# Performance work log

Hardware: AMD Instinct MI355X
Metric: run time of the kernel (lower is better)

The kernel has to match this reference:

```python
import jax, jax.numpy as jnp
import numpy as np

OBS = 128; N_AGENT = 16; N_ACTION = 8; N_LAYER = 2; HID = 128
GE = 256; LE = 256; F1 = 512; F2 = 512


def _edges(batch_size, n):
    # all ordered pairs (i, j), i != j, within each sample; GCNConv adds self-loops
    i, j = np.meshgrid(np.arange(n), np.arange(n), indexing='ij')
    m = i != j
    src0, dst0 = i[m], j[m]                      # [n*(n-1)]
    off = (np.arange(batch_size) * n)[:, None]
    src = (src0[None, :] + off).reshape(-1)
    dst = (dst0[None, :] + off).reshape(-1)
    return jnp.asarray(src, jnp.int32), jnp.asarray(dst, jnp.int32)


def setup_inputs() -> dict:
    key = jax.random.key(0)
    ks = jax.random.split(key, 16)
    g = lambda k, shp, fan: jax.random.normal(k, shp, jnp.float32) / np.sqrt(fan)
    return {
        'obs_j': jax.random.normal(ks[0], (2048, N_AGENT, OBS), jnp.float32),
        'W_pre': g(ks[1], (OBS, HID), OBS), 'b_pre': jnp.zeros((HID,), jnp.float32),
        'W_gcn': g(ks[2], (N_LAYER, HID, HID), HID), 'b_gcn': jnp.zeros((N_LAYER, HID), jnp.float32),
        'W_post': g(ks[3], (HID, GE), HID), 'b_post': jnp.zeros((GE,), jnp.float32),
        'W_loc': g(ks[4], (OBS, LE), OBS), 'b_loc': jnp.zeros((LE,), jnp.float32),
        'W1': g(ks[5], (GE + LE, F1), GE + LE), 'b1': jnp.zeros((F1,), jnp.float32),
        'W2': g(ks[6], (F1, F2), F1), 'b2': jnp.zeros((F2,), jnp.float32),
        'W3': g(ks[7], (F2, N_ACTION), F2), 'b3': jnp.zeros((N_ACTION,), jnp.float32),
    }


def reference(obs_j, W_pre, b_pre, W_gcn, b_gcn, W_post, b_post,
              W_loc, b_loc, W1, b1, W2, b2, W3, b3):
    B, n, _ = obs_j.shape
    N = B * n
    obs = obs_j.reshape(N, OBS)
    x = jax.nn.relu(obs @ W_pre + b_pre)          # [N, HID]

    src, dst = _edges(B, n)
    # GCNConv with self-loops on a fully-connected graph: deg = n for every node,
    # edge norm = 1/sqrt(deg_i*deg_j) = 1/n for every (A+I) edge.
    inv_n = jnp.float32(1.0) / n
    for l in range(N_LAYER):
        h = x @ W_gcn[l]                          # lin (no bias inside propagate)
        agg = jax.ops.segment_sum(h[src], dst, num_segments=N)  # neighbor gather/scatter
        x = jax.nn.relu((agg + h) * inv_n + b_gcn[l])            # + self-loop msg, bias

    g = x.reshape(B, n, HID).mean(axis=1)         # global_mean_pool over each graph
    g = jax.nn.relu(g @ W_post + b_post)          # [B, GE]
    loc = jax.nn.relu(obs @ W_loc + b_loc)        # [B*n, LE]
    gi = jnp.repeat(g, n, axis=0)                 # repeat_interleave over agents
    z = jnp.concatenate([gi, loc], axis=1)
    z = jax.nn.relu(z @ W1 + b1)
    z = jax.nn.relu(z @ W2 + b2)
    q = z @ W3 + b3
    return q.reshape(B, n, N_ACTION)
```

## Files before the change

kernel.cpp:

```cpp
#include <hip/hip_runtime.h>
#include <hip/hip_bf16.h>
#include <stdint.h>

typedef __bf16 bf16;
typedef __bf16 bf16x4 __attribute__((ext_vector_type(4)));
typedef __bf16 bf16x8 __attribute__((ext_vector_type(8)));
typedef float f32x4 __attribute__((ext_vector_type(4)));

#define BM 128
#define BN 128
#define BK 64

#define GL(p) ((const __attribute__((address_space(1))) void*)(p))
#define SH(p) ((__attribute__((address_space(3))) void*)(p))

__device__ inline void tp(const float* W, bf16* WT, int id, int shiftK, int N) {
  int K = 1 << shiftK;
  int n = id >> shiftK;
  int k = id & (K - 1);
  WT[id] = (bf16)W[(size_t)k * N + n];
}

__global__ __launch_bounds__(256) void prep_all(
    const float* __restrict__ obs, bf16* __restrict__ obs_bf,
    const float* __restrict__ W1, const float* __restrict__ W2,
    bf16* __restrict__ W1T, bf16* __restrict__ W2T,
    const float* __restrict__ Wpre, const float* __restrict__ Wloc,
    const float* __restrict__ Wgcn, const float* __restrict__ Wpost,
    bf16* __restrict__ WpreLocT, bf16* __restrict__ Wg0T, bf16* __restrict__ Wg1T,
    bf16* __restrict__ WpostT,
    const float* __restrict__ bpre, const float* __restrict__ bloc,
    float* __restrict__ biasPL) {
  __shared__ bf16 tile[64 * 68];
  int blk = blockIdx.x;
  int tid = threadIdx.x;
  if (blk < 2048) {
    int id = blk * 256 + tid;
    const float4* s = (const float4*)(obs + (size_t)id * 8);
    float4 f0 = s[0], f1 = s[1];
    bf16x8 v;
    v[0] = (bf16)f0.x; v[1] = (bf16)f0.y; v[2] = (bf16)f0.z; v[3] = (bf16)f0.w;
    v[4] = (bf16)f1.x; v[5] = (bf16)f1.y; v[6] = (bf16)f1.z; v[7] = (bf16)f1.w;
    *(bf16x8*)(obs_bf + (size_t)id * 8) = v;
    return;
  }
  blk -= 2048;
  if (blk < 128) {
    const float* W = (blk < 64) ? W1 : W2;
    bf16* WT = (blk < 64) ? W1T : W2T;
    int t = blk & 63;
    int tk0 = (t >> 3) * 64, tn0 = (t & 7) * 64;
#pragma unroll
    for (int p = 0; p < 4; p++) {
      int kr = p * 16 + (tid >> 4), nc = (tid & 15) * 4;
      float4 f = *(const float4*)(W + (size_t)(tk0 + kr) * 512 + tn0 + nc);
      bf16x4 v; v[0] = (bf16)f.x; v[1] = (bf16)f.y; v[2] = (bf16)f.z; v[3] = (bf16)f.w;
      *(bf16x4*)&tile[kr * 68 + nc] = v;
    }
    __syncthreads();
#pragma unroll
    for (int p = 0; p < 4; p++) {
      int nr = p * 16 + (tid >> 4), kc = (tid & 15) * 4;
      bf16x4 v;
#pragma unroll
      for (int i = 0; i < 4; i++) v[i] = tile[(kc + i) * 68 + nr];
      *(bf16x4*)(WT + (size_t)(tn0 + nr) * 512 + tk0 + kc) = v;
    }
    return;
  }
  blk -= 128;
  if (blk < 448) {
    int id = blk * 256 + tid;
    if (id < 16384) { tp(Wpre, WpreLocT, id, 7, 128); return; } id -= 16384;
    if (id < 32768) { tp(Wloc, WpreLocT + 16384, id, 7, 256); return; } id -= 32768;
    if (id < 16384) { tp(Wgcn, Wg0T, id, 7, 128); return; } id -= 16384;
    if (id < 16384) { tp(Wgcn + 16384, Wg1T, id, 7, 128); return; } id -= 16384;
    tp(Wpost, WpostT, id, 7, 256);
    return;
  }
  if (tid < 128) biasPL[tid] = bpre[tid];
  biasPL[128 + tid] = bloc[tid];
}

template <int NT, bool CONCAT, bool POOL, bool QFUSE>
__global__ __launch_bounds__(256, 4) void gemm_k(
    const bf16* __restrict__ Ab, const bf16* __restrict__ Ag,
    const bf16* __restrict__ BT, const float* __restrict__ bias,
    bf16* __restrict__ C, int ldc, bf16* __restrict__ pool_out,
    const float* __restrict__ W3, float* __restrict__ qpart,
    int M, int K) {
  __shared__ bf16 smem[16384];
  bf16* As = smem;
  bf16* Bs = smem + 8192;

  const int tid = threadIdx.x;
  const int id = blockIdx.x;
  const int s = id >> 3;
  const int n_idx = s % NT;
  const int m0 = ((id & 7) + 8 * (s / NT)) * BM;
  const int n0 = n_idx * BN;

  f32x4 acc[4][4] = {};

  const int lane = tid & 63;
  const int wave = tid >> 6;
  const int wm = (wave >> 1) * 64;
  const int wn = (wave & 1) * 64;
  const int lm = lane & 15;
  const int quad = lane >> 4;

  for (int k0 = 0; k0 < K; k0 += BK) {
#pragma unroll
    for (int it = 0; it < 4; it++) {
      int idx = it * 256 + tid;
      int row = idx >> 3;
      int cv8 = (idx & 7) ^ (row & 7);
      int kk = k0 + cv8 * 8;
      const bf16* ga;
      if (CONCAT) {
        int r = m0 + row;
        ga = (k0 < 256) ? (Ag + (size_t)(r >> 4) * 256 + kk)
                        : (Ab + (size_t)r * 256 + (kk - 256));
      } else {
        ga = Ab + (size_t)(m0 + row) * K + kk;
      }
      const bf16* gb = BT + (size_t)(n0 + row) * K + kk;
      __builtin_amdgcn_global_load_lds(GL(ga), SH(&As[(idx & ~63) * 8]), 16, 0, 0);
      __builtin_amdgcn_global_load_lds(GL(gb), SH(&Bs[(idx & ~63) * 8]), 16, 0, 0);
    }
    __syncthreads();

#pragma unroll
    for (int ks = 0; ks < 2; ks++) {
      const int ua = quad + ks * 4;
      bf16x8 a[4], b[4];
#pragma unroll
      for (int i = 0; i < 4; i++) {
        int r = wm + lm + i * 16;
        a[i] = *(const bf16x8*)&As[r * 64 + ((ua ^ (r & 7)) * 8)];
      }
#pragma unroll
      for (int j = 0; j < 4; j++) {
        int r = wn + lm + j * 16;
        b[j] = *(const bf16x8*)&Bs[r * 64 + ((ua ^ (r & 7)) * 8)];
      }
#pragma unroll
      for (int i = 0; i < 4; i++)
#pragma unroll
        for (int j = 0; j < 4; j++)
          acc[i][j] = __builtin_amdgcn_mfma_f32_16x16x32_bf16(a[i], b[j], acc[i][j], 0, 0, 0);
    }
    __syncthreads();
  }

  if (POOL && n_idx == 0) {
#pragma unroll
    for (int i = 0; i < 4; i++) {
      int sample = (m0 + wm + i * 16) >> 4;
#pragma unroll
      for (int j = 0; j < 4; j++) {
        int col = wn + j * 16 + lm;
        float b = bias[col];
        float v = 0.f;
#pragma unroll
        for (int r = 0; r < 4; r++) v += fmaxf(acc[i][j][r] + b, 0.f);
        v += __shfl_xor(v, 16);
        v += __shfl_xor(v, 32);
        if (quad == 0) pool_out[(size_t)sample * 128 + col] = (bf16)(v * 0.0625f);
      }
    }
  } else if (QFUSE) {
#pragma unroll
    for (int i = 0; i < 4; i++)
#pragma unroll
      for (int j = 0; j < 4; j++) {
        int col = wn + j * 16 + lm;
        float b = bias[n0 + col];
#pragma unroll
        for (int r = 0; r < 4; r++) {
          int row = wm + i * 16 + quad * 4 + r;
          smem[row * 128 + col] = (bf16)fmaxf(acc[i][j][r] + b, 0.f);
        }
      }
    __syncthreads();
    int n = lane & 7;
    int kg = lane >> 3;
    float w3r[16];
#pragma unroll
    for (int i = 0; i < 16; i++) w3r[i] = W3[(size_t)(n0 + kg * 16 + i) * 8 + n];
    int rbase = wave * 32;
    for (int rr = 0; rr < 32; rr++) {
      const bf16* zr = &smem[(rbase + rr) * 128 + kg * 16];
      bf16x8 z0 = *(const bf16x8*)zr;
      bf16x8 z1v = *(const bf16x8*)(zr + 8);
      float v = 0.f;
#pragma unroll
      for (int i = 0; i < 8; i++) v += (float)z0[i] * w3r[i];
#pragma unroll
      for (int i = 0; i < 8; i++) v += (float)z1v[i] * w3r[8 + i];
      v += __shfl_down(v, 32);
      v += __shfl_down(v, 16);
      v += __shfl_down(v, 8);
      if (lane < 8) qpart[((size_t)n_idx * 32768 + m0 + rbase + rr) * 8 + n] = v;
    }
  } else {
#pragma unroll
    for (int i = 0; i < 4; i++)
#pragma unroll
      for (int j = 0; j < 4; j++) {
        int col = wn + j * 16 + lm;
        float b = bias[n0 + col];
#pragma unroll
        for (int r = 0; r < 4; r++) {
          int row = wm + i * 16 + quad * 4 + r;
          smem[row * 128 + col] = (bf16)fmaxf(acc[i][j][r] + b, 0.f);
        }
      }
    __syncthreads();
    const int coff = POOL ? (n0 - 128) : n0;
#pragma unroll
    for (int c = 0; c < 8; c++) {
      int ci = c * 256 + tid;
      int row = ci >> 4, col8 = (ci & 15) * 8;
      *(bf16x8*)&C[(size_t)(m0 + row) * ldc + coff + col8] = *(const bf16x8*)&smem[row * 128 + col8];
    }
  }
}

__global__ __launch_bounds__(256) void gcn_chain(
    const bf16* __restrict__ xbar, const bf16* __restrict__ Wg0T,
    const bf16* __restrict__ Wg1T, const bf16* __restrict__ WpostT,
    const float* __restrict__ b_gcn, const float* __restrict__ b_post,
    bf16* __restrict__ g) {
  __shared__ bf16 xs[16 * 136];
  __shared__ bf16 ws[256 * 136];
  const int tid = threadIdx.x;
  const int lane = tid & 63, wave = tid >> 6;
  const int lm = lane & 15, quad = lane >> 4;
  const int rb = blockIdx.x * 16;

  {
    int row = tid >> 4, cv = (tid & 15) * 8;
    *(bf16x8*)&xs[row * 136 + cv] = *(const bf16x8*)&xbar[(size_t)(rb + row) * 128 + cv];
  }

  const bf16* Wl[3] = {Wg0T, Wg1T, WpostT};
  const float* bl[3] = {b_gcn, b_gcn + 128, b_post};
  const int Nl[3] = {128, 128, 256};

  for (int l = 0; l < 3; l++) {
    const int N = Nl[l];
    __syncthreads();
    for (int c = tid; c < N * 16; c += 256) {
      int row = c >> 4, cv = (c & 15) * 8;
      *(bf16x8*)&ws[row * 136 + cv] = *(const bf16x8*)&Wl[l][(size_t)row * 128 + cv];
    }
    __syncthreads();
    const int nj = N / 64;
    f32x4 acc[4] = {};
#pragma unroll
    for (int kk = 0; kk < 128; kk += 32) {
      bf16x8 a = *(const bf16x8*)&xs[lm * 136 + quad * 8 + kk];
      for (int j = 0; j < nj; j++) {
        int col = (wave * nj + j) * 16 + lm;
        bf16x8 b = *(const bf16x8*)&ws[col * 136 + quad * 8 + kk];
        acc[j] = __builtin_amdgcn_mfma_f32_16x16x32_bf16(a, b, acc[j], 0, 0, 0);
      }
    }
    __syncthreads();
    const float* bias = bl[l];
    if (l < 2) {
      for (int j = 0; j < nj; j++) {
        int col = (wave * nj + j) * 16 + lm;
        float bv = bias[col];
#pragma unroll
        for (int r = 0; r < 4; r++)
          xs[(quad * 4 + r) * 136 + col] = (bf16)fmaxf(acc[j][r] + bv, 0.f);
      }
    } else {
      for (int j = 0; j < nj; j++) {
        int col = (wave * nj + j) * 16 + lm;
        float bv = bias[col];
#pragma unroll
        for (int r = 0; r < 4; r++)
          g[(size_t)(rb + quad * 4 + r) * 256 + col] = (bf16)fmaxf(acc[j][r] + bv, 0.f);
      }
    }
  }
}

__global__ __launch_bounds__(256) void reduce_q(const float* __restrict__ qpart,
                                                const float* __restrict__ b3,
                                                float* __restrict__ out) {
  int idx = blockIdx.x * 256 + threadIdx.x;
  const float4* qp = (const float4*)qpart;
  float4 v = qp[idx];
  float4 t1 = qp[idx + 65536];
  float4 t2 = qp[idx + 131072];
  float4 t3 = qp[idx + 196608];
  const float4* b = (const float4*)b3;
  float4 bb = b[idx & 1];
  v.x += t1.x + t2.x + t3.x + bb.x;
  v.y += t1.y + t2.y + t3.y + bb.y;
  v.z += t1.z + t2.z + t3.z + bb.z;
  v.w += t1.w + t2.w + t3.w + bb.w;
  ((float4*)out)[idx] = v;
}

extern "C" void kernel_launch(void* const* d_in, const int* in_sizes, int n_in,
                              void* d_out, int out_size, void* d_ws, size_t ws_size,
                              hipStream_t stream) {
  const float* obs    = (const float*)d_in[0];
  const float* W_pre  = (const float*)d_in[1];
  const float* b_pre  = (const float*)d_in[2];
  const float* W_gcn  = (const float*)d_in[3];
  const float* b_gcn  = (const float*)d_in[4];
  const float* W_post = (const float*)d_in[5];
  const float* b_post = (const float*)d_in[6];
  const float* W_loc  = (const float*)d_in[7];
  const float* b_loc  = (const float*)d_in[8];
  const float* W1     = (const float*)d_in[9];
  const float* b1     = (const float*)d_in[10];
  const float* W2     = (const float*)d_in[11];
  const float* b2     = (const float*)d_in[12];
  const float* W3     = (const float*)d_in[13];
  const float* b3     = (const float*)d_in[14];
  float* out = (float*)d_out;

  char* p = (char*)d_ws;
  auto alloc = [&](size_t bytes) { char* r = p; p += (bytes + 255) & ~(size_t)255; return r; };
  bf16* WpreLocT = (bf16*)alloc(384 * 128 * 2);
  float* biasPL  = (float*)alloc(384 * 4);
  bf16* Wg0T   = (bf16*)alloc(128 * 128 * 2);
  bf16* Wg1T   = (bf16*)alloc(128 * 128 * 2);
  bf16* WpostT = (bf16*)alloc(256 * 128 * 2);
  bf16* W1T    = (bf16*)alloc(512 * 512 * 2);
  bf16* W2T    = (bf16*)alloc(512 * 512 * 2);
  bf16* obs_bf = (bf16*)alloc((size_t)32768 * 128 * 2);
  bf16* xbar   = (bf16*)alloc(2048 * 128 * 2);
  bf16* loc    = (bf16*)alloc((size_t)32768 * 256 * 2);
  bf16* g      = (bf16*)alloc(2048 * 256 * 2);
  bf16* z1     = (bf16*)alloc((size_t)32768 * 512 * 2);
  float* qpart = (float*)alloc((size_t)4 * 32768 * 8 * 4);

  prep_all<<<2625, 256, 0, stream>>>(obs, obs_bf, W1, W2, W1T, W2T,
                                     W_pre, W_loc, W_gcn, W_post,
                                     WpreLocT, Wg0T, Wg1T, WpostT,
                                     b_pre, b_loc, biasPL);
  gemm_k<3, false, true, false><<<768, 256, 0, stream>>>(
      obs_bf, nullptr, WpreLocT, biasPL, loc, 256, xbar, nullptr, nullptr, 32768, 128);
  gcn_chain<<<128, 256, 0, stream>>>(xbar, Wg0T, Wg1T, WpostT, b_gcn, b_post, g);
  gemm_k<4, true, false, false><<<1024, 256, 0, stream>>>(
      loc, g, W1T, b1, z1, 512, nullptr, nullptr, nullptr, 32768, 512);
  gemm_k<4, false, false, true><<<1024, 256, 0, stream>>>(
      z1, nullptr, W2T, b2, nullptr, 0, nullptr, W3, qpart, 32768, 512);
  reduce_q<<<256, 256, 0, stream>>>(qpart, b3, out);
}
```

Measured before the change: 177.4 us.

## Fuse obs bf16 conversion into first GEMM and replace q reduction with atomics

The first GEMM now reads fp32 obs directly, converts it to bf16 in registers and writes it into LDS, so the separate obs_bf pass and its buffer go away. The final Q projection accumulates its per-N-tile partials into the output with atomicAdd, adding b3 from tile 0, instead of writing qpart and running a reduce_q kernel. The output is zeroed by extra blocks in prep_all. The trade-off is that A loads in the first GEMM become synchronous register loads instead of direct-to-LDS loads, and the float atomics make the summation order nondeterministic.

```diff
diff --git a/kernel.cpp b/kernel.cpp
--- a/kernel.cpp
+++ b/kernel.cpp
@@ -22,7 +22,6 @@
 }
 
 __global__ __launch_bounds__(256) void prep_all(
-    const float* __restrict__ obs, bf16* __restrict__ obs_bf,
     const float* __restrict__ W1, const float* __restrict__ W2,
     bf16* __restrict__ W1T, bf16* __restrict__ W2T,
     const float* __restrict__ Wpre, const float* __restrict__ Wloc,
@@ -30,21 +29,10 @@
     bf16* __restrict__ WpreLocT, bf16* __restrict__ Wg0T, bf16* __restrict__ Wg1T,
     bf16* __restrict__ WpostT,
     const float* __restrict__ bpre, const float* __restrict__ bloc,
-    float* __restrict__ biasPL) {
+    float* __restrict__ biasPL, float* __restrict__ outq) {
   __shared__ bf16 tile[64 * 68];
   int blk = blockIdx.x;
   int tid = threadIdx.x;
-  if (blk < 2048) {
-    int id = blk * 256 + tid;
-    const float4* s = (const float4*)(obs + (size_t)id * 8);
-    float4 f0 = s[0], f1 = s[1];
-    bf16x8 v;
-    v[0] = (bf16)f0.x; v[1] = (bf16)f0.y; v[2] = (bf16)f0.z; v[3] = (bf16)f0.w;
-    v[4] = (bf16)f1.x; v[5] = (bf16)f1.y; v[6] = (bf16)f1.z; v[7] = (bf16)f1.w;
-    *(bf16x8*)(obs_bf + (size_t)id * 8) = v;
-    return;
-  }
-  blk -= 2048;
   if (blk < 128) {
     const float* W = (blk < 64) ? W1 : W2;
     bf16* WT = (blk < 64) ? W1T : W2T;
@@ -78,16 +66,25 @@
     tp(Wpost, WpostT, id, 7, 256);
     return;
   }
-  if (tid < 128) biasPL[tid] = bpre[tid];
-  biasPL[128 + tid] = bloc[tid];
-}
-
-template <int NT, bool CONCAT, bool POOL, bool QFUSE>
+  blk -= 448;
+  if (blk == 0) {
+    if (tid < 128) biasPL[tid] = bpre[tid];
+    biasPL[128 + tid] = bloc[tid];
+    return;
+  }
+  blk -= 1;
+  float4 z = {0.f, 0.f, 0.f, 0.f};
+#pragma unroll
+  for (int i = 0; i < 4; i++)
+    ((float4*)outq)[(size_t)blk * 1024 + i * 256 + tid] = z;
+}
+
+template <int NT, int ASRC, bool POOL, bool QFUSE>
 __global__ __launch_bounds__(256, 4) void gemm_k(
-    const bf16* __restrict__ Ab, const bf16* __restrict__ Ag,
+    const float* __restrict__ Af, const bf16* __restrict__ Ab, const bf16* __restrict__ Ag,
     const bf16* __restrict__ BT, const float* __restrict__ bias,
     bf16* __restrict__ C, int ldc, bf16* __restrict__ pool_out,
-    const float* __restrict__ W3, float* __restrict__ qpart,
+    const float* __restrict__ W3, const float* __restrict__ b3, float* __restrict__ outq,
     int M, int K) {
   __shared__ bf16 smem[16384];
   bf16* As = smem;
@@ -114,18 +111,29 @@
     for (int it = 0; it < 4; it++) {
       int idx = it * 256 + tid;
       int row = idx >> 3;
-      int cv8 = (idx & 7) ^ (row & 7);
+      int c = idx & 7;
+      int cv8 = c ^ (row & 7);
       int kk = k0 + cv8 * 8;
-      const bf16* ga;
-      if (CONCAT) {
-        int r = m0 + row;
-        ga = (k0 < 256) ? (Ag + (size_t)(r >> 4) * 256 + kk)
-                        : (Ab + (size_t)r * 256 + (kk - 256));
+      if (ASRC == 1) {
+        const float* src = Af + (size_t)(m0 + row) * K + kk;
+        float4 f0 = *(const float4*)src;
+        float4 f1 = *(const float4*)(src + 4);
+        bf16x8 v;
+        v[0] = (bf16)f0.x; v[1] = (bf16)f0.y; v[2] = (bf16)f0.z; v[3] = (bf16)f0.w;
+        v[4] = (bf16)f1.x; v[5] = (bf16)f1.y; v[6] = (bf16)f1.z; v[7] = (bf16)f1.w;
+        *(bf16x8*)&As[row * 64 + c * 8] = v;
       } else {
-        ga = Ab + (size_t)(m0 + row) * K + kk;
+        const bf16* ga;
+        if (ASRC == 2) {
+          int r = m0 + row;
+          ga = (k0 < 256) ? (Ag + (size_t)(r >> 4) * 256 + kk)
+                          : (Ab + (size_t)r * 256 + (kk - 256));
+        } else {
+          ga = Ab + (size_t)(m0 + row) * K + kk;
+        }
+        __builtin_amdgcn_global_load_lds(GL(ga), SH(&As[(idx & ~63) * 8]), 16, 0, 0);
       }
       const bf16* gb = BT + (size_t)(n0 + row) * K + kk;
-      __builtin_amdgcn_global_load_lds(GL(ga), SH(&As[(idx & ~63) * 8]), 16, 0, 0);
       __builtin_amdgcn_global_load_lds(GL(gb), SH(&Bs[(idx & ~63) * 8]), 16, 0, 0);
     }
     __syncthreads();
@@ -188,6 +196,7 @@
     float w3r[16];
 #pragma unroll
     for (int i = 0; i < 16; i++) w3r[i] = W3[(size_t)(n0 + kg * 16 + i) * 8 + n];
+    float bn = (n_idx == 0) ? b3[n] : 0.f;
     int rbase = wave * 32;
     for (int rr = 0; rr < 32; rr++) {
       const bf16* zr = &smem[(rbase + rr) * 128 + kg * 16];
@@ -201,7 +210,7 @@
       v += __shfl_down(v, 32);
       v += __shfl_down(v, 16);
       v += __shfl_down(v, 8);
-      if (lane < 8) qpart[((size_t)n_idx * 32768 + m0 + rbase + rr) * 8 + n] = v;
+      if (lane < 8) atomicAdd(&outq[(size_t)(m0 + rbase + rr) * 8 + n], v + bn);
     }
   } else {
 #pragma unroll
@@ -287,24 +296,6 @@
       }
     }
   }
-}
-
-__global__ __launch_bounds__(256) void reduce_q(const float* __restrict__ qpart,
-                                                const float* __restrict__ b3,
-                                                float* __restrict__ out) {
-  int idx = blockIdx.x * 256 + threadIdx.x;
-  const float4* qp = (const float4*)qpart;
-  float4 v = qp[idx];
-  float4 t1 = qp[idx + 65536];
-  float4 t2 = qp[idx + 131072];
-  float4 t3 = qp[idx + 196608];
-  const float4* b = (const float4*)b3;
-  float4 bb = b[idx & 1];
-  v.x += t1.x + t2.x + t3.x + bb.x;
-  v.y += t1.y + t2.y + t3.y + bb.y;
-  v.z += t1.z + t2.z + t3.z + bb.z;
-  v.w += t1.w + t2.w + t3.w + bb.w;
-  ((float4*)out)[idx] = v;
 }
 
 extern "C" void kernel_launch(void* const* d_in, const int* in_sizes, int n_in,
@@ -336,23 +327,23 @@
   bf16* WpostT = (bf16*)alloc(256 * 128 * 2);
   bf16* W1T    = (bf16*)alloc(512 * 512 * 2);
   bf16* W2T    = (bf16*)alloc(512 * 512 * 2);
-  bf16* obs_bf = (bf16*)alloc((size_t)32768 * 128 * 2);
   bf16* xbar   = (bf16*)alloc(2048 * 128 * 2);
   bf16* loc    = (bf16*)alloc((size_t)32768 * 256 * 2);
   bf16* g      = (bf16*)alloc(2048 * 256 * 2);
   bf16* z1     = (bf16*)alloc((size_t)32768 * 512 * 2);
-  float* qpart = (float*)alloc((size_t)4 * 32768 * 8 * 4);
-
-  prep_all<<<2625, 256, 0, stream>>>(obs, obs_bf, W1, W2, W1T, W2T,
-                                     W_pre, W_loc, W_gcn, W_post,
-                                     WpreLocT, Wg0T, Wg1T, WpostT,
-                                     b_pre, b_loc, biasPL);
-  gemm_k<3, false, true, false><<<768, 256, 0, stream>>>(
-      obs_bf, nullptr, WpreLocT, biasPL, loc, 256, xbar, nullptr, nullptr, 32768, 128);
+
+  prep_all<<<641, 256, 0, stream>>>(W1, W2, W1T, W2T,
+                                    W_pre, W_loc, W_gcn, W_post,
+                                    WpreLocT, Wg0T, Wg1T, WpostT,
+                                    b_pre, b_loc, biasPL, out);
+  gemm_k<3, 1, true, false><<<768, 256, 0, stream>>>(
+      obs, nullptr, nullptr, WpreLocT, biasPL, loc, 256, xbar,
+      nullptr, nullptr, nullptr, 32768, 128);
   gcn_chain<<<128, 256, 0, stream>>>(xbar, Wg0T, Wg1T, WpostT, b_gcn, b_post, g);
-  gemm_k<4, true, false, false><<<1024, 256, 0, stream>>>(
-      loc, g, W1T, b1, z1, 512, nullptr, nullptr, nullptr, 32768, 512);
-  gemm_k<4, false, false, true><<<1024, 256, 0, stream>>>(
-      z1, nullptr, W2T, b2, nullptr, 0, nullptr, W3, qpart, 32768, 512);
-  reduce_q<<<256, 256, 0, stream>>>(qpart, b3, out);
-}
+  gemm_k<4, 2, false, false><<<1024, 256, 0, stream>>>(
+      nullptr, loc, g, W1T, b1, z1, 512, nullptr,
+      nullptr, nullptr, nullptr, 32768, 512);
+  gemm_k<4, 0, false, true><<<1024, 256, 0, stream>>>(
+      nullptr, z1, nullptr, W2T, b2, nullptr, 0, nullptr,
+      W3, b3, out, 32768, 512);
+}
```

Measured after the change: 174.3 us. About the same (-1.8%).
